# Performance work log

Hardware: AMD Instinct MI355X
Metric: run time of the kernel (lower is better)

## Reference

```python
import jax, jax.numpy as jnp
import numpy as np

SAMPLE_RATE = 44100.0
MIN_GAIN, MAX_GAIN = -12.0, 12.0
MIN_Q, MAX_Q = 0.1, 10.0
# (min, max) for the 15 normalized control params, in channel order
PARAM_RANGES = np.array([
    (MIN_GAIN, MAX_GAIN), (20.0, 2000.0), (MIN_Q, MAX_Q),      # low shelf
    (MIN_GAIN, MAX_GAIN), (20.0, 200.0), (MIN_Q, MAX_Q),       # band0 peaking
    (MIN_GAIN, MAX_GAIN), (200.0, 2000.0), (MIN_Q, MAX_Q),     # band1 peaking
    (MIN_GAIN, MAX_GAIN), (2000.0, 12000.0), (MIN_Q, MAX_Q),   # band2 peaking
    (MIN_GAIN, MAX_GAIN), (4000.0, 16000.0), (MIN_Q, MAX_Q),   # high shelf
], dtype=np.float32)


def _biquad(gain_db, f0, q, ftype):
    """RBJ cookbook biquad. Inputs shape (bs,), returns (bs, 6) normalized so a0==1."""
    A = 10.0 ** (gain_db / 40.0)
    w0 = 2.0 * jnp.pi * (f0 / SAMPLE_RATE)
    alpha = jnp.sin(w0) / (2.0 * q)
    cw = jnp.cos(w0)
    sA = jnp.sqrt(A)
    if ftype == 'peaking':
        b0 = 1.0 + alpha * A; b1 = -2.0 * cw; b2 = 1.0 - alpha * A
        a0 = 1.0 + alpha / A; a1 = -2.0 * cw; a2 = 1.0 - alpha / A
    elif ftype == 'low_shelf':
        b0 = A * ((A + 1) - (A - 1) * cw + 2 * sA * alpha)
        b1 = 2 * A * ((A - 1) - (A + 1) * cw)
        b2 = A * ((A + 1) - (A - 1) * cw - 2 * sA * alpha)
        a0 = (A + 1) + (A - 1) * cw + 2 * sA * alpha
        a1 = -2 * ((A - 1) + (A + 1) * cw)
        a2 = (A + 1) + (A - 1) * cw - 2 * sA * alpha
    else:  # high_shelf
        b0 = A * ((A + 1) + (A - 1) * cw + 2 * sA * alpha)
        b1 = -2 * A * ((A - 1) + (A + 1) * cw)
        b2 = A * ((A + 1) + (A - 1) * cw - 2 * sA * alpha)
        a0 = (A + 1) - (A - 1) * cw + 2 * sA * alpha
        a1 = 2 * ((A - 1) - (A + 1) * cw)
        a2 = (A + 1) - (A - 1) * cw - 2 * sA * alpha
    coeffs = jnp.stack([b0, b1, b2, a0, a1, a2], axis=-1)
    return coeffs / a0[..., None]


def _compute_sos(p):
    """p: (bs, 15) denormalized params -> sos (bs, 5, 6)."""
    secs = [
        _biquad(p[:, 0], p[:, 1], p[:, 2], 'low_shelf'),
        _biquad(p[:, 3], p[:, 4], p[:, 5], 'peaking'),
        _biquad(p[:, 6], p[:, 7], p[:, 8], 'peaking'),
        _biquad(p[:, 9], p[:, 10], p[:, 11], 'peaking'),
        _biquad(p[:, 12], p[:, 13], p[:, 14], 'high_shelf'),
    ]
    return jnp.stack(secs, axis=1)


def _sosfilt(sos, x):
    """Cascaded 5-section biquad, direct form II transposed, zero initial state.
    sos: (bs, 5, 6), x: (bs, T) -> (bs, T)."""
    b0, b1, b2 = sos[..., 0], sos[..., 1], sos[..., 2]  # each (bs, 5)
    a1, a2 = sos[..., 4], sos[..., 5]

    def step(carry, xt):
        z1, z2 = carry  # (bs, 5) each
        s = xt  # (bs,)
        z1n, z2n = [], []
        for k in range(5):  # fixed small cascade
            y = b0[:, k] * s + z1[:, k]
            z1n.append(b1[:, k] * s - a1[:, k] * y + z2[:, k])
            z2n.append(b2[:, k] * s - a2[:, k] * y)
            s = y
        return (jnp.stack(z1n, 1), jnp.stack(z2n, 1)), s

    bs = x.shape[0]
    z0 = jnp.zeros((bs, 5), x.dtype)
    _, y = jax.lax.scan(step, (z0, z0), x.T)
    return y.T


def setup_inputs() -> dict:
    key = jax.random.key(0)
    k1, k2 = jax.random.split(key)
    x = jax.random.normal(k1, (32, 1, 131072), dtype=jnp.float32)
    control_params = jax.random.uniform(k2, (32, 15, 1), dtype=jnp.float32)
    return {"x": x, "control_params": control_params}


def reference(x, control_params):
    # denormalize: min + p * (max - min)
    lo = jnp.asarray(PARAM_RANGES[:, 0])
    hi = jnp.asarray(PARAM_RANGES[:, 1])
    p = control_params[:, :, 0]  # (bs, 15)
    p_denorm = lo[None, :] + p * (hi - lo)[None, :]
    sos = _compute_sos(p_denorm)           # (bs, 5, 6)
    y = _sosfilt(sos, x[:, 0, :])          # (bs, T)
    return y[:, None, :], sos
```

## Files before the change

### kernel.cpp

```cpp
#include <hip/hip_runtime.h>
#include <math.h>


#define NB 32
#define LCH 32
#define T_LEN 131072
#define CPB 256
#define SPB 16
#define NPOW 12
#define PROW 12

__constant__ double c_lo[15] = {-12.0,   20.0, 0.1,
                                -12.0,   20.0, 0.1,
                                -12.0,  200.0, 0.1,
                                -12.0, 2000.0, 0.1,
                                -12.0, 4000.0, 0.1};
__constant__ double c_hi[15] = { 12.0,  2000.0, 10.0,
                                 12.0,   200.0, 10.0,
                                 12.0,  2000.0, 10.0,
                                 12.0, 12000.0, 10.0,
                                 12.0, 16000.0, 10.0};

__global__ __launch_bounds__(128)
void eq_setup(const float* __restrict__ cp, float* __restrict__ sos_out,
              float* __restrict__ powers, unsigned int* __restrict__ flags)
{
    int b = blockIdx.x;
    int t = threadIdx.x;
    __shared__ float  sc[5][5];
    __shared__ double Abuf[2][10][10];

    if (t < SPB) flags[b * SPB + t] = 0u;

    if (t < 5) {
        int k = t;
        double p[3];
#pragma unroll
        for (int j = 0; j < 3; ++j) {
            int i = k * 3 + j;
            double pv = (double)cp[b * 15 + i];
            p[j] = c_lo[i] + pv * (c_hi[i] - c_lo[i]);
        }
        double A     = exp(p[0] * (M_LN10 / 40.0));
        double w0    = 2.0 * M_PI * p[1] / 44100.0;
        double alpha = sin(w0) / (2.0 * p[2]);
        double cw    = cos(w0);
        double sA    = sqrt(A);
        double b0, b1, b2, a0, a1, a2;
        if (k == 0) {
            b0 =     A * ((A + 1) - (A - 1) * cw + 2 * sA * alpha);
            b1 = 2 * A * ((A - 1) - (A + 1) * cw);
            b2 =     A * ((A + 1) - (A - 1) * cw - 2 * sA * alpha);
            a0 =          (A + 1) + (A - 1) * cw + 2 * sA * alpha;
            a1 =    -2 * ((A - 1) + (A + 1) * cw);
            a2 =          (A + 1) + (A - 1) * cw - 2 * sA * alpha;
        } else if (k == 4) {
            b0 =     A * ((A + 1) + (A - 1) * cw + 2 * sA * alpha);
            b1 = -2 * A * ((A - 1) + (A + 1) * cw);
            b2 =     A * ((A + 1) + (A - 1) * cw - 2 * sA * alpha);
            a0 =          (A + 1) - (A - 1) * cw + 2 * sA * alpha;
            a1 =     2 * ((A - 1) - (A + 1) * cw);
            a2 =          (A + 1) - (A - 1) * cw - 2 * sA * alpha;
        } else {
            b0 = 1.0 + alpha * A;
            b1 = -2.0 * cw;
            b2 = 1.0 - alpha * A;
            a0 = 1.0 + alpha / A;
            a1 = -2.0 * cw;
            a2 = 1.0 - alpha / A;
        }
        double inv = 1.0 / a0;
        float fb0 = (float)(b0 * inv), fb1 = (float)(b1 * inv), fb2 = (float)(b2 * inv);
        float fa1 = (float)(a1 * inv), fa2 = (float)(a2 * inv);
        float* o = sos_out + (size_t)(b * 5 + k) * 6;
        o[0] = fb0; o[1] = fb1; o[2] = fb2; o[3] = 1.0f; o[4] = fa1; o[5] = fa2;
        sc[k][0] = fb0; sc[k][1] = fb1; sc[k][2] = fb2; sc[k][3] = fa1; sc[k][4] = fa2;
    }
    __syncthreads();

    if (t < 10) {
        double z[10];
#pragma unroll
        for (int i = 0; i < 10; ++i) z[i] = 0.0;
        z[t] = 1.0;
        double s = 0.0;
        double zn[10];
#pragma unroll
        for (int k = 0; k < 5; ++k) {
            double b0 = sc[k][0], b1 = sc[k][1], b2 = sc[k][2];
            double a1 = sc[k][3], a2 = sc[k][4];
            double y = b0 * s + z[2 * k];
            zn[2 * k]     = b1 * s - a1 * y + z[2 * k + 1];
            zn[2 * k + 1] = b2 * s - a2 * y;
            s = y;
        }
#pragma unroll
        for (int r = 0; r < 10; ++r) Abuf[0][r][t] = zn[r];
    }
    __syncthreads();

    int r = t / 10, cc = t % 10;
    int cur = 0;
    for (int sq = 0; sq < 16; ++sq) {
        double acc = 0.0;
        if (t < 100) {
#pragma unroll
            for (int j = 0; j < 10; ++j) acc += Abuf[cur][r][j] * Abuf[cur][j][cc];
        }
        __syncthreads();
        if (t < 100) Abuf[cur ^ 1][r][cc] = acc;
        __syncthreads();
        cur ^= 1;
        if (sq >= 4 && t < 100) {
            int m = sq - 4;
            powers[((size_t)b * NPOW + m) * 100 + t] = (float)Abuf[cur][r][cc];
        }
    }
}

template<bool ACC>
__device__ __forceinline__ void affineL(const float* __restrict__ P,
                                        const float u[PROW], float v[10])
{
#pragma unroll
    for (int rr = 0; rr < 10; ++rr) {
        const float* rp = P + rr * PROW;
        float a = ACC ? v[rr] : 0.0f;
#pragma unroll
        for (int c = 0; c < PROW; ++c) a = fmaf(rp[c], u[c], a);
        v[rr] = a;
    }
}

__device__ __forceinline__ void matvecL(const float* __restrict__ P, float v[10])
{
    float u[PROW];
#pragma unroll
    for (int i = 0; i < 10; ++i) u[i] = v[i];
    u[10] = 0.0f; u[11] = 0.0f;
    affineL<false>(P, u, v);
}

__global__ __launch_bounds__(256, 2)
void eq_main(const float* __restrict__ x, const float* __restrict__ sos,
             const float* __restrict__ powers, float* __restrict__ agg,
             unsigned int* __restrict__ flags, float* __restrict__ y)
{
    int blk = blockIdx.x;
    int b = blk >> 4, sp = blk & (SPB - 1);
    int tid = threadIdx.x;
    int w = tid >> 6, lw = tid & 63;

    __shared__ float Pl[NPOW * 10 * PROW];
    __shared__ float wt[4][10];
    __shared__ float Sseed[10];

    {
        const float* src = powers + (size_t)b * NPOW * 100;
        for (int i = tid; i < NPOW * 10 * PROW; i += 256) {
            int c = i % PROW;
            int r = (i / PROW) % 10;
            int m = i / (10 * PROW);
            Pl[i] = (c < 10) ? src[m * 100 + r * 10 + c] : 0.0f;
        }
    }

    const float* s5 = sos + (size_t)(b * 5) * 6;
    float cb0[5], cb1[5], cb2[5], ca1[5], ca2[5];
#pragma unroll
    for (int k = 0; k < 5; ++k) {
        cb0[k] = s5[k * 6 + 0]; cb1[k] = s5[k * 6 + 1]; cb2[k] = s5[k * 6 + 2];
        ca1[k] = s5[k * 6 + 4]; ca2[k] = s5[k * 6 + 5];
    }

    int c = sp * CPB + tid;
    const float* xp = x + (size_t)b * T_LEN + (size_t)c * LCH;
    float xr[LCH];
#pragma unroll
    for (int t0 = 0; t0 < LCH; t0 += 4) {
        float4 xv = *reinterpret_cast<const float4*>(xp + t0);
        xr[t0] = xv.x; xr[t0 + 1] = xv.y; xr[t0 + 2] = xv.z; xr[t0 + 3] = xv.w;
    }

    float z1[5] = {0, 0, 0, 0, 0}, z2[5] = {0, 0, 0, 0, 0};
#pragma unroll
    for (int j = 0; j < LCH; ++j) {
        float s = xr[j];
#pragma unroll
        for (int k = 0; k < 5; ++k) {
            float yk = fmaf(cb0[k], s, z1[k]);
            float u  = fmaf(cb1[k], s, z2[k]);
            z1[k] = fmaf(-ca1[k], yk, u);
            z2[k] = fmaf(-ca2[k], yk, cb2[k] * s);
            s = yk;
        }
    }
    float sv[10];
#pragma unroll
    for (int k = 0; k < 5; ++k) { sv[2 * k] = z1[k]; sv[2 * k + 1] = z2[k]; }

    __syncthreads();

#pragma unroll
    for (int j = 0; j < 6; ++j) {
        const float* P = Pl + j * 10 * PROW;
        float u[PROW];
#pragma unroll
        for (int i = 0; i < 10; ++i) u[i] = __shfl_up(sv[i], 1 << j);
        u[10] = 0.0f; u[11] = 0.0f;
        if (lw >= (1 << j)) affineL<true>(P, u, sv);
    }
    float es[10];
#pragma unroll
    for (int i = 0; i < 10; ++i) es[i] = __shfl_up(sv[i], 1);
    if (lw == 0) {
#pragma unroll
        for (int i = 0; i < 10; ++i) es[i] = 0.0f;
    }
    if (lw == 63) {
#pragma unroll
        for (int i = 0; i < 10; ++i) wt[w][i] = sv[i];
    }
    __syncthreads();

    if (tid == 0) {
        float E[10];
#pragma unroll
        for (int i = 0; i < 10; ++i) E[i] = wt[0][i];
#pragma unroll
        for (int j = 1; j < 4; ++j) {
            matvecL(Pl + 6 * 10 * PROW, E);
#pragma unroll
            for (int i = 0; i < 10; ++i) E[i] += wt[j][i];
        }
        float* ap = agg + (size_t)(b * SPB + sp) * 10;
#pragma unroll
        for (int i = 0; i < 10; ++i)
            __hip_atomic_store(&ap[i], E[i], __ATOMIC_RELAXED, __HIP_MEMORY_SCOPE_AGENT);
        __hip_atomic_store(&flags[b * SPB + sp], 1u, __ATOMIC_RELEASE,
                           __HIP_MEMORY_SCOPE_AGENT);
    }

    if (w == 0) {
        float tv[10];
#pragma unroll
        for (int i = 0; i < 10; ++i) tv[i] = 0.0f;
        if (lw < SPB) {
            while (__hip_atomic_load(&flags[b * SPB + lw], __ATOMIC_ACQUIRE,
                                     __HIP_MEMORY_SCOPE_AGENT) == 0u) {
                __builtin_amdgcn_s_sleep(1);
            }
            const float* ap = agg + (size_t)(b * SPB + lw) * 10;
#pragma unroll
            for (int i = 0; i < 10; ++i)
                tv[i] = __hip_atomic_load(&ap[i], __ATOMIC_RELAXED,
                                          __HIP_MEMORY_SCOPE_AGENT);
        }
#pragma unroll
        for (int j = 0; j < 4; ++j) {
            const float* P = Pl + (8 + j) * 10 * PROW;
            float u[PROW];
#pragma unroll
            for (int i = 0; i < 10; ++i) u[i] = __shfl_up(tv[i], 1 << j);
            u[10] = 0.0f; u[11] = 0.0f;
            if (lw >= (1 << j) && lw < SPB) affineL<true>(P, u, tv);
        }
        float sd[10];
#pragma unroll
        for (int i = 0; i < 10; ++i) sd[i] = __shfl(tv[i], (sp - 1) & 63);
        if (sp == 0) {
#pragma unroll
            for (int i = 0; i < 10; ++i) sd[i] = 0.0f;
        }
        if (lw == 0) {
#pragma unroll
            for (int i = 0; i < 10; ++i) Sseed[i] = sd[i];
        }
    }
    __syncthreads();

    float F[10];
#pragma unroll
    for (int i = 0; i < 10; ++i) F[i] = Sseed[i];
    if (w & 1) matvecL(Pl + 6 * 10 * PROW, F);
    if (w & 2) matvecL(Pl + 7 * 10 * PROW, F);
    {
        float Ew[10];
#pragma unroll
        for (int i = 0; i < 10; ++i) Ew[i] = 0.0f;
        for (int j = 0; j < w; ++j) {
            matvecL(Pl + 6 * 10 * PROW, Ew);
#pragma unroll
            for (int i = 0; i < 10; ++i) Ew[i] += wt[j][i];
        }
#pragma unroll
        for (int i = 0; i < 10; ++i) F[i] += Ew[i];
    }
#pragma unroll
    for (int m = 0; m < 6; ++m) {
        if ((lw >> m) & 1) matvecL(Pl + m * 10 * PROW, F);
    }
#pragma unroll
    for (int k = 0; k < 5; ++k) {
        z1[k] = F[2 * k]     + es[2 * k];
        z2[k] = F[2 * k + 1] + es[2 * k + 1];
    }

    float* yp = y + (size_t)b * T_LEN + (size_t)c * LCH;
#pragma unroll
    for (int t0 = 0; t0 < LCH; t0 += 4) {
        float o4[4];
#pragma unroll
        for (int j = 0; j < 4; ++j) {
            float s = xr[t0 + j];
#pragma unroll
            for (int k = 0; k < 5; ++k) {
                float yk = fmaf(cb0[k], s, z1[k]);
                float u  = fmaf(cb1[k], s, z2[k]);
                z1[k] = fmaf(-ca1[k], yk, u);
                z2[k] = fmaf(-ca2[k], yk, cb2[k] * s);
                s = yk;
            }
            o4[j] = s;
        }
        *reinterpret_cast<float4*>(yp + t0) = make_float4(o4[0], o4[1], o4[2], o4[3]);
    }
}

extern "C" void kernel_launch(void* const* d_in, const int* in_sizes, int n_in,
                              void* d_out, int out_size, void* d_ws, size_t ws_size,
                              hipStream_t stream)
{
    const float* x  = (const float*)d_in[0];
    const float* cp = (const float*)d_in[1];
    float* out = (float*)d_out;
    float* sos = out + (size_t)NB * T_LEN;

    float*        powers = (float*)d_ws;
    float*        agg    = powers + (size_t)NB * NPOW * 100;
    unsigned int* flags  = (unsigned int*)(agg + (size_t)NB * SPB * 10);

    eq_setup<<<dim3(NB), dim3(128), 0, stream>>>(cp, sos, powers, flags);
    eq_main<<<dim3(NB * SPB), dim3(256), 0, stream>>>(x, sos, powers, agg, flags, out);
}
```

Baseline: 49.19 us.

## Halve chunk length, double blocks per batch, exploit triangular transition matrices

Cuts the per-thread chunk from 32 to 16 samples and doubles the blocks per batch row to 32. One more matrix power is computed to cover the deeper cross-block scan, and launch bounds are raised so more blocks fit per CU. The state-transition matvecs now skip the known-zero upper-triangular entries of the cascade's block-lower-triangular matrix, cutting FMAs in the scan. In exchange the scan overhead grows relative to the shorter sequential work, and more blocks must be co-resident for the spin-wait flag protocol.

```diff
diff --git a/kernel.cpp b/kernel.cpp
--- a/kernel.cpp
+++ b/kernel.cpp
@@ -3,12 +3,13 @@
 
 
 #define NB 32
-#define LCH 32
+#define LCH 16
 #define T_LEN 131072
 #define CPB 256
-#define SPB 16
-#define NPOW 12
+#define SPB 32
+#define NPOW 13
 #define PROW 12
+#define PMAT (10 * PROW)
 
 __constant__ double c_lo[15] = {-12.0,   20.0, 0.1,
                                 -12.0,   20.0, 0.1,
@@ -111,56 +112,55 @@
         if (t < 100) Abuf[cur ^ 1][r][cc] = acc;
         __syncthreads();
         cur ^= 1;
-        if (sq >= 4 && t < 100) {
-            int m = sq - 4;
+        if (sq >= 3 && t < 100) {
+            int m = sq - 3;
             powers[((size_t)b * NPOW + m) * 100 + t] = (float)Abuf[cur][r][cc];
         }
     }
 }
 
 template<bool ACC>
-__device__ __forceinline__ void affineL(const float* __restrict__ P,
-                                        const float u[PROW], float v[10])
+__device__ __forceinline__ void affineT(const float* __restrict__ P,
+                                        const float u[10], float v[10])
 {
 #pragma unroll
     for (int rr = 0; rr < 10; ++rr) {
         const float* rp = P + rr * PROW;
         float a = ACC ? v[rr] : 0.0f;
 #pragma unroll
-        for (int c = 0; c < PROW; ++c) a = fmaf(rp[c], u[c], a);
+        for (int c = 0; c <= (rr | 1); ++c) a = fmaf(rp[c], u[c], a);
         v[rr] = a;
     }
 }
 
-__device__ __forceinline__ void matvecL(const float* __restrict__ P, float v[10])
-{
-    float u[PROW];
+__device__ __forceinline__ void matvecT(const float* __restrict__ P, float v[10])
+{
+    float u[10];
 #pragma unroll
     for (int i = 0; i < 10; ++i) u[i] = v[i];
-    u[10] = 0.0f; u[11] = 0.0f;
-    affineL<false>(P, u, v);
-}
-
-__global__ __launch_bounds__(256, 2)
+    affineT<false>(P, u, v);
+}
+
+__global__ __launch_bounds__(256, 4)
 void eq_main(const float* __restrict__ x, const float* __restrict__ sos,
              const float* __restrict__ powers, float* __restrict__ agg,
              unsigned int* __restrict__ flags, float* __restrict__ y)
 {
     int blk = blockIdx.x;
-    int b = blk >> 4, sp = blk & (SPB - 1);
+    int b = blk >> 5, sp = blk & (SPB - 1);
     int tid = threadIdx.x;
     int w = tid >> 6, lw = tid & 63;
 
-    __shared__ float Pl[NPOW * 10 * PROW];
+    __shared__ float Pl[NPOW * PMAT];
     __shared__ float wt[4][10];
     __shared__ float Sseed[10];
 
     {
         const float* src = powers + (size_t)b * NPOW * 100;
-        for (int i = tid; i < NPOW * 10 * PROW; i += 256) {
+        for (int i = tid; i < NPOW * PMAT; i += 256) {
             int c = i % PROW;
             int r = (i / PROW) % 10;
-            int m = i / (10 * PROW);
+            int m = i / PMAT;
             Pl[i] = (c < 10) ? src[m * 100 + r * 10 + c] : 0.0f;
         }
     }
@@ -203,12 +203,11 @@
 
 #pragma unroll
     for (int j = 0; j < 6; ++j) {
-        const float* P = Pl + j * 10 * PROW;
-        float u[PROW];
+        const float* P = Pl + j * PMAT;
+        float u[10];
 #pragma unroll
         for (int i = 0; i < 10; ++i) u[i] = __shfl_up(sv[i], 1 << j);
-        u[10] = 0.0f; u[11] = 0.0f;
-        if (lw >= (1 << j)) affineL<true>(P, u, sv);
+        if (lw >= (1 << j)) affineT<true>(P, u, sv);
     }
     float es[10];
 #pragma unroll
@@ -229,7 +228,7 @@
         for (int i = 0; i < 10; ++i) E[i] = wt[0][i];
 #pragma unroll
         for (int j = 1; j < 4; ++j) {
-            matvecL(Pl + 6 * 10 * PROW, E);
+            matvecT(Pl + 6 * PMAT, E);
 #pragma unroll
             for (int i = 0; i < 10; ++i) E[i] += wt[j][i];
         }
@@ -248,7 +247,7 @@
         if (lw < SPB) {
             while (__hip_atomic_load(&flags[b * SPB + lw], __ATOMIC_ACQUIRE,
                                      __HIP_MEMORY_SCOPE_AGENT) == 0u) {
-                __builtin_amdgcn_s_sleep(1);
+                __builtin_amdgcn_s_sleep(2);
             }
             const float* ap = agg + (size_t)(b * SPB + lw) * 10;
 #pragma unroll
@@ -257,13 +256,12 @@
                                           __HIP_MEMORY_SCOPE_AGENT);
         }
 #pragma unroll
-        for (int j = 0; j < 4; ++j) {
-            const float* P = Pl + (8 + j) * 10 * PROW;
-            float u[PROW];
+        for (int j = 0; j < 5; ++j) {
+            const float* P = Pl + (8 + j) * PMAT;
+            float u[10];
 #pragma unroll
             for (int i = 0; i < 10; ++i) u[i] = __shfl_up(tv[i], 1 << j);
-            u[10] = 0.0f; u[11] = 0.0f;
-            if (lw >= (1 << j) && lw < SPB) affineL<true>(P, u, tv);
+            if (lw >= (1 << j) && lw < SPB) affineT<true>(P, u, tv);
         }
         float sd[10];
 #pragma unroll
@@ -282,14 +280,14 @@
     float F[10];
 #pragma unroll
     for (int i = 0; i < 10; ++i) F[i] = Sseed[i];
-    if (w & 1) matvecL(Pl + 6 * 10 * PROW, F);
-    if (w & 2) matvecL(Pl + 7 * 10 * PROW, F);
+    if (w & 1) matvecT(Pl + 6 * PMAT, F);
+    if (w & 2) matvecT(Pl + 7 * PMAT, F);
     {
         float Ew[10];
 #pragma unroll
         for (int i = 0; i < 10; ++i) Ew[i] = 0.0f;
         for (int j = 0; j < w; ++j) {
-            matvecL(Pl + 6 * 10 * PROW, Ew);
+            matvecT(Pl + 6 * PMAT, Ew);
 #pragma unroll
             for (int i = 0; i < 10; ++i) Ew[i] += wt[j][i];
         }
@@ -298,7 +296,7 @@
     }
 #pragma unroll
     for (int m = 0; m < 6; ++m) {
-        if ((lw >> m) & 1) matvecL(Pl + m * 10 * PROW, F);
+        if ((lw >> m) & 1) matvecT(Pl + m * PMAT, F);
     }
 #pragma unroll
     for (int k = 0; k < 5; ++k) {
```

After: 68.19 us. 1.39x slower.
